# Optimization experiments

Hardware: AMD Instinct MI355X
Metric: run time of the kernel (lower is better)

Reference implementation:

```python
import jax, jax.numpy as jnp
import numpy as np

NUM_HEADS = 8
NUM_LAYER = 4


def setup_inputs() -> dict:
    key = jax.random.key(0)
    k1, k2, k3, k4, k5, k6, k7 = jax.random.split(key, 7)
    bs, num, C = 2, 2048, 256
    H0 = (jax.random.uniform(k1, (bs, num, num)) < 0.3).astype(jnp.float32)
    vertex_feat = jax.random.normal(k2, (bs, C, num), dtype=jnp.float32)
    edge_feat = jax.random.normal(k3, (bs, C, num), dtype=jnp.float32)
    s = 1.0 / np.sqrt(C)
    # Conv1d(kernel_size=1) weights, squeezed to [C_out, C_in]
    Wq = jax.random.uniform(k4, (C, C), minval=-s, maxval=s, dtype=jnp.float32)
    bq = jax.random.uniform(k5, (C,), minval=-s, maxval=s, dtype=jnp.float32)
    Wk = jax.random.uniform(k6, (C, C), minval=-s, maxval=s, dtype=jnp.float32)
    bk = jax.random.uniform(k7, (C,), minval=-s, maxval=s, dtype=jnp.float32)
    return {"H0": H0, "vertex_feat": vertex_feat, "edge_feat": edge_feat,
            "Wq": Wq, "bq": bq, "Wk": Wk, "bk": bk, "iter": 1}


def reference(H0, vertex_feat, edge_feat, Wq, bq, Wk, bk, iter):
    bs, num, _ = H0.shape
    C = vertex_feat.shape[1]
    h = NUM_HEADS
    d = C // h
    # 1x1 Conv1d == per-position linear; reshape to heads: [bs, h, d, num]
    Q = (jnp.einsum('oc,bcn->bon', Wq, vertex_feat) + bq[None, :, None]).reshape(bs, h, d, num)
    K = (jnp.einsum('oc,bcn->bon', Wk, edge_feat) + bk[None, :, None]).reshape(bs, h, d, num)
    attn = jnp.einsum('bhco,bhci->bhoi', Q, K) / np.sqrt(d)  # [bs, h, num, num]
    # attention_mask = (1 - H0).masked_fill((1-H0).bool(), -1e9)
    m = 1.0 - H0
    m = jnp.where(m != 0, jnp.float32(-1e9), m)
    score = jax.nn.sigmoid(attn + m[:, None, :, :]).sum(axis=1) / h  # [bs, num, num]
    # top-k row thresholding (k static: iter is a python int)
    k = max(1, round(num * 0.1 * (NUM_LAYER - 1 - iter)))
    topk_vals = jax.lax.top_k(score, k)[0]           # sorted descending
    a_min = topk_vals[..., -1:]                      # row-wise k-th largest
    W = jnp.where(score >= a_min, score, jnp.float32(0.0))
    H = jnp.where(W > 0, H0, jnp.float32(0.0))
    # degree normalizations (1e-10 keeps them finite; torch isinf branch is a no-op)
    De_n_1 = (1.0 / (H.sum(axis=1) + 1e-10))[..., None]  # [bs, num, 1]
    Dv_n_1 = (1.0 / (H.sum(axis=2) + 1e-10))[..., None]  # [bs, num, 1]
    # F.normalize(W.sum(dim=1), dim=1): L2 normalize with eps=1e-12
    W_edge = W.sum(axis=1)
    W_edge = W_edge / jnp.maximum(jnp.linalg.norm(W_edge, axis=1, keepdims=True), 1e-12)
    W_edge = W_edge[..., None]  # [bs, num, 1]
    return (H, W, De_n_1, Dv_n_1, W_edge)
```

## Files before the change

### kernel.cpp

```cpp
#include <hip/hip_runtime.h>
#include <math.h>

#define NUM 2048
#define CDIM 256
#define NUM_LAYER 4

typedef _Float16 f16x8 __attribute__((ext_vector_type(8)));
typedef unsigned short u16x8 __attribute__((ext_vector_type(8)));
typedef float f32x4 __attribute__((ext_vector_type(4)));

static __device__ __forceinline__ void split_f16(float x, unsigned short& h,
                                                 unsigned short& l) {
  _Float16 hi = (_Float16)x;
  float r = x - (float)hi;
  _Float16 lo = (_Float16)r;
  h = __builtin_bit_cast(unsigned short, hi);
  l = __builtin_bit_cast(unsigned short, lo);
}

static __device__ __forceinline__ void split3_f16(float x, unsigned short& h,
                                                  unsigned short& m,
                                                  unsigned short& l) {
  float xh = (fabsf(x) >= 6.103515625e-05f) ? x : 0.0f;
  _Float16 hi = (_Float16)xh;
  float r1 = x - (float)hi;
  float r1s = r1 * 2048.0f;
  _Float16 mi = (_Float16)r1s;
  float r2s = (r1s - (float)mi) * 2048.0f;
  _Float16 lo = (_Float16)r2s;
  h = __builtin_bit_cast(unsigned short, hi);
  m = __builtin_bit_cast(unsigned short, mi);
  l = __builtin_bit_cast(unsigned short, lo);
}

__global__ __launch_bounds__(256) void proj_kernel(
    const float* __restrict__ Wq, const float* __restrict__ bq,
    const float* __restrict__ Wk, const float* __restrict__ bk,
    const float* __restrict__ vf, const float* __restrict__ ef,
    unsigned short* __restrict__ Qhi, unsigned short* __restrict__ Qlo,
    unsigned short* __restrict__ Khi, unsigned short* __restrict__ Klo)
{
  const int z = blockIdx.z;
  const int b = z >> 1, mm2 = z & 1;
  const float* __restrict__ Wmat = mm2 ? Wk : Wq;
  const float* __restrict__ bias = mm2 ? bk : bq;
  const float* __restrict__ x = (mm2 ? ef : vf) + (size_t)b * CDIM * NUM;
  unsigned short* __restrict__ ohi = mm2 ? Khi : Qhi;
  unsigned short* __restrict__ olo = mm2 ? Klo : Qlo;

  const int n0 = blockIdx.x * 64;
  const int o0 = blockIdx.y * 64;

  __shared__ unsigned short xsh[3][64][36];
  __shared__ unsigned short wsh[3][64][36];
  __shared__ float T[64][69];

  const int t = threadIdx.x, lane = t & 63, wave = t >> 6;
  const int ml = lane & 15, quad = lane >> 4;
  const int nbl = wave * 16;

  const int cp = t >> 4;
  const int nq = t & 15;
  const int orow = t >> 2;
  const int cq = (t & 3) * 8;

  f32x4 acc0[4], acc1[4], acc2[4];
  #pragma unroll
  for (int ot = 0; ot < 4; ot++) {
    acc0[ot] = (f32x4){0.f, 0.f, 0.f, 0.f};
    acc1[ot] = (f32x4){0.f, 0.f, 0.f, 0.f};
    acc2[ot] = (f32x4){0.f, 0.f, 0.f, 0.f};
  }

  for (int cc = 0; cc < CDIM; cc += 32) {
    if (cc) __syncthreads();
    {
      const float4 f4a = *(const float4*)&x[(size_t)(cc + 2*cp) * NUM + n0 + nq*4];
      const float4 f4b = *(const float4*)&x[(size_t)(cc + 2*cp + 1) * NUM + n0 + nq*4];
      const float va[4] = {f4a.x, f4a.y, f4a.z, f4a.w};
      const float vb[4] = {f4b.x, f4b.y, f4b.z, f4b.w};
      #pragma unroll
      for (int j = 0; j < 4; j++) {
        unsigned short h0, m0, l0, h1, m1, l1;
        split3_f16(va[j], h0, m0, l0);
        split3_f16(vb[j], h1, m1, l1);
        *(unsigned*)&xsh[0][nq*4 + j][2*cp] = (unsigned)h0 | ((unsigned)h1 << 16);
        *(unsigned*)&xsh[1][nq*4 + j][2*cp] = (unsigned)m0 | ((unsigned)m1 << 16);
        *(unsigned*)&xsh[2][nq*4 + j][2*cp] = (unsigned)l0 | ((unsigned)l1 << 16);
      }
    }
    {
      const float4 w0 = *(const float4*)&Wmat[(size_t)(o0 + orow) * CDIM + cc + cq];
      const float4 w1 = *(const float4*)&Wmat[(size_t)(o0 + orow) * CDIM + cc + cq + 4];
      const float wv[8] = {w0.x, w0.y, w0.z, w0.w, w1.x, w1.y, w1.z, w1.w};
      #pragma unroll
      for (int j = 0; j < 4; j++) {
        unsigned short h0, m0, l0, h1, m1, l1;
        split3_f16(wv[2*j],   h0, m0, l0);
        split3_f16(wv[2*j+1], h1, m1, l1);
        *(unsigned*)&wsh[0][orow][cq + 2*j] = (unsigned)h0 | ((unsigned)h1 << 16);
        *(unsigned*)&wsh[1][orow][cq + 2*j] = (unsigned)m0 | ((unsigned)m1 << 16);
        *(unsigned*)&wsh[2][orow][cq + 2*j] = (unsigned)l0 | ((unsigned)l1 << 16);
      }
    }
    __syncthreads();
    const f16x8 bh = *(const f16x8*)&xsh[0][nbl + ml][quad*8];
    const f16x8 bm = *(const f16x8*)&xsh[1][nbl + ml][quad*8];
    const f16x8 bl = *(const f16x8*)&xsh[2][nbl + ml][quad*8];
    #pragma unroll
    for (int ot = 0; ot < 4; ot++) {
      const f16x8 ah = *(const f16x8*)&wsh[0][ot*16 + ml][quad*8];
      const f16x8 am = *(const f16x8*)&wsh[1][ot*16 + ml][quad*8];
      const f16x8 al = *(const f16x8*)&wsh[2][ot*16 + ml][quad*8];
      acc0[ot] = __builtin_amdgcn_mfma_f32_16x16x32_f16(ah, bh, acc0[ot], 0, 0, 0);
      acc1[ot] = __builtin_amdgcn_mfma_f32_16x16x32_f16(ah, bm, acc1[ot], 0, 0, 0);
      acc1[ot] = __builtin_amdgcn_mfma_f32_16x16x32_f16(am, bh, acc1[ot], 0, 0, 0);
      acc2[ot] = __builtin_amdgcn_mfma_f32_16x16x32_f16(ah, bl, acc2[ot], 0, 0, 0);
      acc2[ot] = __builtin_amdgcn_mfma_f32_16x16x32_f16(al, bh, acc2[ot], 0, 0, 0);
      acc2[ot] = __builtin_amdgcn_mfma_f32_16x16x32_f16(am, bm, acc2[ot], 0, 0, 0);
    }
  }

  const float S1 = 4.8828125e-04f;
  const float S2 = 2.38418579101562e-07f;
  #pragma unroll
  for (int ot = 0; ot < 4; ot++)
    #pragma unroll
    for (int r = 0; r < 4; r++)
      T[nbl + ml][ot*16 + quad*4 + r] =
          acc0[ot][r] + S1 * acc1[ot][r] + S2 * acc2[ot][r];
  __syncthreads();

  const float SC = -1.4426950408889634f * 0.17677669529663687f;
  const float osc = mm2 ? 1.0f : SC;
  const int n_l = t >> 2;
  const int oc  = (t & 3) * 16;
  float xv[16];
  #pragma unroll
  for (int j = 0; j < 4; j++) {
    const float4 bj = *(const float4*)&bias[o0 + oc + j*4];
    xv[j*4+0] = (T[n_l][oc + j*4+0] + bj.x) * osc;
    xv[j*4+1] = (T[n_l][oc + j*4+1] + bj.y) * osc;
    xv[j*4+2] = (T[n_l][oc + j*4+2] + bj.z) * osc;
    xv[j*4+3] = (T[n_l][oc + j*4+3] + bj.w) * osc;
  }
  unsigned short hi[16], lo[16];
  #pragma unroll
  for (int j = 0; j < 16; j++) split_f16(xv[j], hi[j], lo[j]);
  const size_t gb = ((size_t)b * NUM + n0 + n_l) * CDIM + o0 + oc;
  *(u16x8*)&ohi[gb]   = *(u16x8*)&hi[0];
  *(u16x8*)&ohi[gb+8] = *(u16x8*)&hi[8];
  *(u16x8*)&olo[gb]   = *(u16x8*)&lo[0];
  *(u16x8*)&olo[gb+8] = *(u16x8*)&lo[8];
}

__global__ __launch_bounds__(512, 2) void score_kernel(
    const unsigned short* __restrict__ Qhi, const unsigned short* __restrict__ Qlo,
    const unsigned short* __restrict__ Khi, const unsigned short* __restrict__ Klo,
    float* __restrict__ score)
{
  const int b = blockIdx.z;
  const int i0 = blockIdx.x * 128;
  const int o0 = blockIdx.y * 128;
  const int t = threadIdx.x, lane = t & 63, wave = t >> 6;
  const int m = lane & 15, quad = lane >> 4;
  const int obl = (wave & 1) * 64;
  const int ibl = (wave >> 1) * 32;

  __shared__ unsigned short qsh[2][2][128][36];
  __shared__ unsigned short ksh[2][2][128][36];

  const int srow = t >> 2;
  const int schk = (t & 3) * 8;
  const size_t gq = ((size_t)b * NUM + o0 + srow) * CDIM + schk;
  const size_t gk = ((size_t)b * NUM + i0 + srow) * CDIM + schk;

  f32x4 ssum[4][2];
  #pragma unroll
  for (int a = 0; a < 4; a++)
    #pragma unroll
    for (int c = 0; c < 2; c++) ssum[a][c] = (f32x4){0.f, 0.f, 0.f, 0.f};

  u16x8 pq[2], pk[2];
  pq[0] = *(const u16x8*)&Qhi[gq];
  pq[1] = *(const u16x8*)&Qlo[gq];
  pk[0] = *(const u16x8*)&Khi[gk];
  pk[1] = *(const u16x8*)&Klo[gk];
  *(u16x8*)&qsh[0][0][srow][schk] = pq[0];
  *(u16x8*)&qsh[0][1][srow][schk] = pq[1];
  *(u16x8*)&ksh[0][0][srow][schk] = pk[0];
  *(u16x8*)&ksh[0][1][srow][schk] = pk[1];
  __syncthreads();
  pq[0] = *(const u16x8*)&Qhi[gq + 32];
  pq[1] = *(const u16x8*)&Qlo[gq + 32];
  pk[0] = *(const u16x8*)&Khi[gk + 32];
  pk[1] = *(const u16x8*)&Klo[gk + 32];

  for (int h = 0; h < 8; h++) {
    const int c = h & 1;
    f16x8 a[4][2], bb[2][2];
    #pragma unroll
    for (int ot = 0; ot < 4; ot++)
      #pragma unroll
      for (int cp = 0; cp < 2; cp++)
        a[ot][cp] = *(const f16x8*)&qsh[c][cp][obl + ot*16 + m][quad*8];
    #pragma unroll
    for (int it = 0; it < 2; it++)
      #pragma unroll
      for (int cp = 0; cp < 2; cp++)
        bb[it][cp] = *(const f16x8*)&ksh[c][cp][ibl + it*16 + m][quad*8];

    __builtin_amdgcn_s_setprio(1);
    #pragma unroll
    for (int it = 0; it < 2; it++) {
      #pragma unroll
      for (int ot = 0; ot < 4; ot++) {
        f32x4 cc = (f32x4){0.f, 0.f, 0.f, 0.f};
        cc = __builtin_amdgcn_mfma_f32_16x16x32_f16(a[ot][0], bb[it][0], cc, 0, 0, 0);
        cc = __builtin_amdgcn_mfma_f32_16x16x32_f16(a[ot][0], bb[it][1], cc, 0, 0, 0);
        cc = __builtin_amdgcn_mfma_f32_16x16x32_f16(a[ot][1], bb[it][0], cc, 0, 0, 0);
        #pragma unroll
        for (int r = 0; r < 4; r++)
          ssum[ot][it][r] += __builtin_amdgcn_rcpf(1.0f + __builtin_amdgcn_exp2f(cc[r]));
      }
    }
    __builtin_amdgcn_s_setprio(0);

    if (h < 7) {
      *(u16x8*)&qsh[c^1][0][srow][schk] = pq[0];
      *(u16x8*)&qsh[c^1][1][srow][schk] = pq[1];
      *(u16x8*)&ksh[c^1][0][srow][schk] = pk[0];
      *(u16x8*)&ksh[c^1][1][srow][schk] = pk[1];
      __syncthreads();
      if (h < 6) {
        const size_t co = (size_t)(h + 2) * 32;
        pq[0] = *(const u16x8*)&Qhi[gq + co];
        pq[1] = *(const u16x8*)&Qlo[gq + co];
        pk[0] = *(const u16x8*)&Khi[gk + co];
        pk[1] = *(const u16x8*)&Klo[gk + co];
      }
    }
  }

  const int ob = o0 + obl, ib = i0 + ibl;
  #pragma unroll
  for (int ot = 0; ot < 4; ot++)
    #pragma unroll
    for (int it = 0; it < 2; it++)
      #pragma unroll
      for (int r = 0; r < 4; r++) {
        const int row = ob + ot*16 + quad*4 + r;
        const int col = ib + it*16 + m;
        const size_t idx = ((size_t)b * NUM + row) * NUM + col;
        score[idx] = ssum[ot][it][r] * 0.125f;
      }
}

__global__ __launch_bounds__(256) void topk_apply_kernel(
    float* __restrict__ scoreW, const float* __restrict__ H0,
    float* __restrict__ Hout, const int* __restrict__ iterp,
    float* __restrict__ DvOut)
{
  const int wave = threadIdx.x >> 6, lane = threadIdx.x & 63;
  const int row = blockIdx.x * 4 + wave;
  __shared__ unsigned int hist_all[4][256];
  unsigned int* __restrict__ h = hist_all[wave];
  unsigned int* __restrict__ srow = (unsigned int*)scoreW + (size_t)row * NUM;
  const float* __restrict__ h0row = H0 + (size_t)row * NUM;
  float* __restrict__ Hrow = Hout + (size_t)row * NUM;

  uint4 v[8];
  #pragma unroll
  for (int q = 0; q < 8; q++) {
    const uint4 s4 = ((const uint4*)srow)[lane + 64*q];
    const float4 m4 = ((const float4*)h0row)[lane + 64*q];
    v[q].x = (m4.x != 0.0f) ? s4.x : 0u;
    v[q].y = (m4.y != 0.0f) ? s4.y : 0u;
    v[q].z = (m4.z != 0.0f) ? s4.z : 0u;
    v[q].w = (m4.w != 0.0f) ? s4.w : 0u;
  }

  const int it = iterp[0];
  int k = (int)((double)NUM * 0.1 * (double)(NUM_LAYER - 1 - it) + 0.5);
  if (k < 1) k = 1;
  if (k > NUM) k = NUM;

  unsigned int prefix = 0;
  unsigned int rem = (unsigned int)k;

  for (int pass = 3; pass >= 0; pass--) {
    const int shift = pass * 8;
    const unsigned int pmask = (pass == 3) ? 0u : (0xFFFFFFFFu << (shift + 8));
    *(uint4*)&h[lane*4] = make_uint4(0u, 0u, 0u, 0u);
    __threadfence_block();
    unsigned int zc = 0;
    #pragma unroll
    for (int q = 0; q < 8; q++) {
      const unsigned int vv[4] = {v[q].x, v[q].y, v[q].z, v[q].w};
      #pragma unroll
      for (int e = 0; e < 4; e++) {
        unsigned int val = vv[e];
        if ((val & pmask) == prefix) {
          unsigned int bin = (val >> shift) & 255u;
          if (bin) atomicAdd(&h[bin], 1u);
          else zc++;
        }
      }
    }
    #pragma unroll
    for (int off = 32; off > 0; off >>= 1) zc += __shfl_down(zc, off, 64);
    if (lane == 0) h[0] = zc;
    __threadfence_block();
    const uint4 T = *(const uint4*)&h[lane*4];
    unsigned int s3 = T.w;
    unsigned int s2 = T.z + s3;
    unsigned int s1 = T.y + s2;
    unsigned int s0 = T.x + s1;
    unsigned int tot = s0;
    #pragma unroll
    for (int off = 1; off < 64; off <<= 1) {
      unsigned int y = __shfl_down(tot, off, 64);
      if (lane + off < 64) tot += y;
    }
    const unsigned int ac = tot - s0;
    const unsigned int cum[4]   = {s0 + ac, s1 + ac, s2 + ac, s3 + ac};
    const unsigned int above[4] = {s1 + ac, s2 + ac, s3 + ac, ac};
    int fq = -1;
    #pragma unroll
    for (int q = 0; q < 4; q++)
      if (cum[q] >= rem && above[q] < rem) fq = q;
    const unsigned long long mask = __ballot(fq >= 0);
    const int src = (int)(__ffsll((long long)mask) - 1);
    const unsigned int selbin = (fq >= 0) ? (unsigned int)(lane*4 + fq) : 0u;
    const unsigned int nrem   = (fq >= 0) ? (rem - above[fq]) : 0u;
    const unsigned int sel = (unsigned int)__shfl((int)selbin, src, 64);
    rem = (unsigned int)__shfl((int)nrem, src, 64);
    prefix |= (sel << shift);
  }

  const unsigned int amin = prefix;
  float cnt = 0.0f;
  #pragma unroll
  for (int q = 0; q < 8; q++) {
    unsigned int w0 = (v[q].x >= amin) ? v[q].x : 0u;
    unsigned int w1 = (v[q].y >= amin) ? v[q].y : 0u;
    unsigned int w2 = (v[q].z >= amin) ? v[q].z : 0u;
    unsigned int w3 = (v[q].w >= amin) ? v[q].w : 0u;
    float h0 = (w0 != 0u) ? 1.0f : 0.0f;
    float h1 = (w1 != 0u) ? 1.0f : 0.0f;
    float h2 = (w2 != 0u) ? 1.0f : 0.0f;
    float h3 = (w3 != 0u) ? 1.0f : 0.0f;
    cnt += h0 + h1 + h2 + h3;
    ((uint4*)srow)[lane + 64*q] = make_uint4(w0, w1, w2, w3);
    ((float4*)Hrow)[lane + 64*q] = make_float4(h0, h1, h2, h3);
  }
  #pragma unroll
  for (int off = 32; off > 0; off >>= 1) cnt += __shfl_down(cnt, off, 64);
  if (lane == 0) DvOut[row] = 1.0f / (cnt + 1e-10f);
}

__global__ __launch_bounds__(256) void colsum_kernel(
    const float* __restrict__ Wmat,
    float* __restrict__ colH, float* __restrict__ colW)
{
  const int b = blockIdx.z;
  const int i = blockIdx.x * 256 + threadIdx.x;
  const int o0 = blockIdx.y * 64;
  float sh = 0.0f, sw = 0.0f;
  for (int o = 0; o < 64; o++) {
    size_t idx = ((size_t)b * NUM + o0 + o) * NUM + i;
    float w = Wmat[idx];
    sw += w;
    sh += (w > 0.0f) ? 1.0f : 0.0f;
  }
  atomicAdd(&colH[b * NUM + i], sh);
  atomicAdd(&colW[b * NUM + i], sw);
}

__global__ __launch_bounds__(1024) void finalize_kernel(
    const float* __restrict__ colH, const float* __restrict__ colW,
    float* __restrict__ De, float* __restrict__ We)
{
  const int b = blockIdx.x;
  const int t = threadIdx.x;
  float cw[2];
  float sq = 0.0f;
  #pragma unroll
  for (int j = 0; j < 2; j++) {
    int i = t + 1024*j;
    float ch = colH[b * NUM + i];
    De[b * NUM + i] = 1.0f / (ch + 1e-10f);
    cw[j] = colW[b * NUM + i];
    sq += cw[j] * cw[j];
  }
  for (int off = 32; off > 0; off >>= 1) sq += __shfl_down(sq, off, 64);
  __shared__ float red[16];
  __shared__ float s_nrm;
  if ((t & 63) == 0) red[t >> 6] = sq;
  __syncthreads();
  if (t == 0) {
    float tot = 0.0f;
    for (int i2 = 0; i2 < 16; i2++) tot += red[i2];
    s_nrm = fmaxf(sqrtf(tot), 1e-12f);
  }
  __syncthreads();
  #pragma unroll
  for (int j = 0; j < 2; j++)
    We[b * NUM + t + 1024*j] = cw[j] / s_nrm;
}

extern "C" void kernel_launch(void* const* d_in, const int* in_sizes, int n_in,
                              void* d_out, int out_size, void* d_ws, size_t ws_size,
                              hipStream_t stream) {
  const float* H0 = (const float*)d_in[0];
  const float* vf = (const float*)d_in[1];
  const float* ef = (const float*)d_in[2];
  const float* Wq = (const float*)d_in[3];
  const float* bq = (const float*)d_in[4];
  const float* Wk = (const float*)d_in[5];
  const float* bk = (const float*)d_in[6];
  const int* iter = (const int*)d_in[7];

  float* out = (float*)d_out;
  const size_t nH = (size_t)2 * NUM * NUM;
  float* Hout  = out;
  float* Wout  = out + nH;
  float* DeOut = out + 2 * nH;
  float* DvOut = DeOut + 2 * NUM;
  float* WeOut = DvOut + 2 * NUM;

  float* colH = (float*)d_ws;
  float* colW = colH + 2 * NUM;

  const size_t nC = (size_t)2 * NUM * CDIM;
  unsigned short* base = (unsigned short*)Hout;
  unsigned short* Qhi = base;
  unsigned short* Qlo = base + nC;
  unsigned short* Khi = base + 2 * nC;
  unsigned short* Klo = base + 3 * nC;

  hipMemsetAsync(d_ws, 0, (size_t)2 * 2 * NUM * sizeof(float), stream);

  proj_kernel<<<dim3(NUM/64, CDIM/64, 4), 256, 0, stream>>>(
      Wq, bq, Wk, bk, vf, ef, Qhi, Qlo, Khi, Klo);
  score_kernel<<<dim3(NUM/128, NUM/128, 2), 512, 0, stream>>>(
      Qhi, Qlo, Khi, Klo, Wout);
  topk_apply_kernel<<<dim3(NUM/2), 256, 0, stream>>>(Wout, H0, Hout, iter, DvOut);
  colsum_kernel<<<dim3(NUM/256, NUM/64, 2), 256, 0, stream>>>(Wout, colH, colW);
  finalize_kernel<<<dim3(2), 1024, 0, stream>>>(colH, colW, DeOut, WeOut);
}
```

Measured before the change: 179.2 us.

## Stage score tile through LDS for coalesced stores; bitwise binary search top-k

The score kernel now writes its MFMA accumulator tile into shared memory (reusing the Q/K staging buffers) and then stores each 128x128 tile to global memory with row-contiguous float4 writes, replacing scattered per-element stores. The top-k threshold search replaces the 4-pass 8-bit radix histogram, which used LDS atomics, with a 32-step bitwise binary search that counts elements at or above a candidate using wave reductions. The first change adds two block barriers and an LDS round trip. The second trades atomic contention for many more compare and shuffle-reduction steps.

```diff
diff --git a/kernel.cpp b/kernel.cpp
--- a/kernel.cpp
+++ b/kernel.cpp
@@ -167,8 +167,9 @@
   const int obl = (wave & 1) * 64;
   const int ibl = (wave >> 1) * 32;
 
-  __shared__ unsigned short qsh[2][2][128][36];
-  __shared__ unsigned short ksh[2][2][128][36];
+  __shared__ __align__(16) unsigned short smem[2][2][2][128][36];
+  #define qsh smem[0]
+  #define ksh smem[1]
 
   const int srow = t >> 2;
   const int schk = (t & 3) * 8;
@@ -242,18 +243,27 @@
     }
   }
 
-  const int ob = o0 + obl, ib = i0 + ibl;
+  __syncthreads();
+  float* Tbuf = (float*)&smem[0][0][0][0][0];
   #pragma unroll
   for (int ot = 0; ot < 4; ot++)
     #pragma unroll
     for (int it = 0; it < 2; it++)
       #pragma unroll
-      for (int r = 0; r < 4; r++) {
-        const int row = ob + ot*16 + quad*4 + r;
-        const int col = ib + it*16 + m;
-        const size_t idx = ((size_t)b * NUM + row) * NUM + col;
-        score[idx] = ssum[ot][it][r] * 0.125f;
-      }
+      for (int r = 0; r < 4; r++)
+        Tbuf[(obl + ot*16 + quad*4 + r) * 132 + ibl + it*16 + m] =
+            ssum[ot][it][r] * 0.125f;
+  __syncthreads();
+  const int r_l = t >> 2;
+  const int c_l = (t & 3) * 32;
+  const size_t gbase = ((size_t)b * NUM + o0 + r_l) * NUM + i0 + c_l;
+  #pragma unroll
+  for (int j = 0; j < 8; j++) {
+    const float4 f4 = *(const float4*)&Tbuf[r_l * 132 + c_l + j*4];
+    *(float4*)&score[gbase + j*4] = f4;
+  }
+  #undef qsh
+  #undef ksh
 }
 
 __global__ __launch_bounds__(256) void topk_apply_kernel(
@@ -263,8 +273,6 @@
 {
   const int wave = threadIdx.x >> 6, lane = threadIdx.x & 63;
   const int row = blockIdx.x * 4 + wave;
-  __shared__ unsigned int hist_all[4][256];
-  unsigned int* __restrict__ h = hist_all[wave];
   unsigned int* __restrict__ srow = (unsigned int*)scoreW + (size_t)row * NUM;
   const float* __restrict__ h0row = H0 + (size_t)row * NUM;
   float* __restrict__ Hrow = Hout + (size_t)row * NUM;
@@ -284,61 +292,26 @@
   int k = (int)((double)NUM * 0.1 * (double)(NUM_LAYER - 1 - it) + 0.5);
   if (k < 1) k = 1;
   if (k > NUM) k = NUM;
-
-  unsigned int prefix = 0;
-  unsigned int rem = (unsigned int)k;
-
-  for (int pass = 3; pass >= 0; pass--) {
-    const int shift = pass * 8;
-    const unsigned int pmask = (pass == 3) ? 0u : (0xFFFFFFFFu << (shift + 8));
-    *(uint4*)&h[lane*4] = make_uint4(0u, 0u, 0u, 0u);
-    __threadfence_block();
-    unsigned int zc = 0;
+  const unsigned int ku = (unsigned int)k;
+
+  unsigned int cur = 0;
+  for (int bit = 31; bit >= 0; bit--) {
+    const unsigned int cand = cur | (1u << bit);
+    unsigned int c = 0;
     #pragma unroll
     for (int q = 0; q < 8; q++) {
-      const unsigned int vv[4] = {v[q].x, v[q].y, v[q].z, v[q].w};
-      #pragma unroll
-      for (int e = 0; e < 4; e++) {
-        unsigned int val = vv[e];
-        if ((val & pmask) == prefix) {
-          unsigned int bin = (val >> shift) & 255u;
-          if (bin) atomicAdd(&h[bin], 1u);
-          else zc++;
-        }
-      }
-    }
-    #pragma unroll
-    for (int off = 32; off > 0; off >>= 1) zc += __shfl_down(zc, off, 64);
-    if (lane == 0) h[0] = zc;
-    __threadfence_block();
-    const uint4 T = *(const uint4*)&h[lane*4];
-    unsigned int s3 = T.w;
-    unsigned int s2 = T.z + s3;
-    unsigned int s1 = T.y + s2;
-    unsigned int s0 = T.x + s1;
-    unsigned int tot = s0;
-    #pragma unroll
-    for (int off = 1; off < 64; off <<= 1) {
-      unsigned int y = __shfl_down(tot, off, 64);
-      if (lane + off < 64) tot += y;
-    }
-    const unsigned int ac = tot - s0;
-    const unsigned int cum[4]   = {s0 + ac, s1 + ac, s2 + ac, s3 + ac};
-    const unsigned int above[4] = {s1 + ac, s2 + ac, s3 + ac, ac};
-    int fq = -1;
-    #pragma unroll
-    for (int q = 0; q < 4; q++)
-      if (cum[q] >= rem && above[q] < rem) fq = q;
-    const unsigned long long mask = __ballot(fq >= 0);
-    const int src = (int)(__ffsll((long long)mask) - 1);
-    const unsigned int selbin = (fq >= 0) ? (unsigned int)(lane*4 + fq) : 0u;
-    const unsigned int nrem   = (fq >= 0) ? (rem - above[fq]) : 0u;
-    const unsigned int sel = (unsigned int)__shfl((int)selbin, src, 64);
-    rem = (unsigned int)__shfl((int)nrem, src, 64);
-    prefix |= (sel << shift);
-  }
-
-  const unsigned int amin = prefix;
+      c += (v[q].x >= cand);
+      c += (v[q].y >= cand);
+      c += (v[q].z >= cand);
+      c += (v[q].w >= cand);
+    }
+    #pragma unroll
+    for (int off = 32; off > 0; off >>= 1) c += __shfl_down(c, off, 64);
+    c = (unsigned int)__shfl((int)c, 0, 64);
+    if (c >= ku) cur = cand;
+  }
+
+  const unsigned int amin = cur;
   float cnt = 0.0f;
   #pragma unroll
   for (int q = 0; q < 8; q++) {
```

After: 200.3 us. 1.12x slower.
